# Kernel tuning notes

Hardware: AMD Instinct MI355X
Metric: run time of the kernel (lower is better)

## Reference

```python
import jax, jax.numpy as jnp
import numpy as np

B, S, H = 64, 256, 768
T, D = 13, 64  # ent_type_size, inner_dim
NEG = 1e12


def setup_inputs() -> dict:
    key = jax.random.key(0)
    k1, k2 = jax.random.split(key)
    return {
        "last_hidden_state": jax.random.normal(k1, (B, S, H), dtype=jnp.float32),
        "dense_w": jax.random.normal(k2, (H, T * 2 * D), dtype=jnp.float32) * (1.0 / np.sqrt(H)),
        "dense_b": jnp.zeros((T * 2 * D,), dtype=jnp.float32),
        "attention_mask": jnp.ones((B, S), dtype=jnp.float32),
    }


def _rope_sin_cos(seq_len, dim, dtype):
    # sinusoidal_position_embedding: even slots sin, odd slots cos
    pos = jnp.arange(seq_len, dtype=dtype)[:, None]                      # [S,1]
    inv = jnp.power(10000.0, -2.0 * jnp.arange(dim // 2, dtype=dtype) / dim)
    ang = pos * inv                                                      # [S,D/2]
    # cos_pos = emb[...,1::2].repeat_interleave(2) ; sin_pos = emb[...,::2].repeat_interleave(2)
    cos_pos = jnp.repeat(jnp.cos(ang), 2, axis=-1)                       # [S,D]
    sin_pos = jnp.repeat(jnp.sin(ang), 2, axis=-1)                       # [S,D]
    return sin_pos, cos_pos


def _rotate(x):
    # stack([-x[...,1::2], x[...,::2]], -1).reshape(x.shape)
    x2 = jnp.stack([-x[..., 1::2], x[..., ::2]], axis=-1)
    return x2.reshape(x.shape)


def reference(last_hidden_state, dense_w, dense_b, attention_mask):
    b, s, _ = last_hidden_state.shape
    out = last_hidden_state @ dense_w + dense_b                          # [B,S,T*2D]
    out = out.reshape(b, s, T, 2 * D)                                    # split+stack
    qw, kw = out[..., :D], out[..., D:]                                  # [B,S,T,D]

    sin_pos, cos_pos = _rope_sin_cos(s, D, out.dtype)
    cosb = cos_pos[None, :, None, :]                                     # [1,S,1,D]
    sinb = sin_pos[None, :, None, :]
    qw = qw * cosb + _rotate(qw) * sinb
    kw = kw * cosb + _rotate(kw) * sinb

    logits = jnp.einsum('bmhd,bnhd->bhmn', qw, kw)                       # [B,T,S,S]

    pad = attention_mask[:, None, None, :]                               # mask over key dim n
    logits = logits * pad - (1.0 - pad) * NEG
    tril = jnp.tril(jnp.ones((s, s), dtype=logits.dtype), -1)            # strict lower tri
    logits = logits - tril * NEG
    return logits / (D ** 0.5)
```

## Files before the change

### kernel.cpp

```cpp
#include <hip/hip_runtime.h>

#define S_LEN 256
#define H_DIM 768
#define T_HEADS 13
#define WN 1664
#define NEGV 1.0e12f

typedef __bf16 bf16x8 __attribute__((ext_vector_type(8)));
typedef float f32x4 __attribute__((ext_vector_type(4)));
typedef float f32x16 __attribute__((ext_vector_type(16)));
typedef unsigned int u32x4 __attribute__((ext_vector_type(4)));
typedef int i32x8 __attribute__((ext_vector_type(8)));

static __device__ __forceinline__ ushort f2bf(float x) {
  unsigned u = __float_as_uint(x);
  return (ushort)((u + 0x7FFFu + ((u >> 16) & 1u)) >> 16);
}

#define GLOAD16(gp, lp)                                                        \
  __builtin_amdgcn_global_load_lds(                                            \
      (const __attribute__((address_space(1))) unsigned int*)(gp),             \
      (__attribute__((address_space(3))) unsigned int*)(lp), 16, 0, 0)

#define PREP_LHS_BLOCKS 6144
#define PREP_WT_BLOCKS 312
#define PREP_ROPE_BLOCKS 16

__global__ __launch_bounds__(256) void prep_all(const float* __restrict__ lhs,
                                                const float* __restrict__ W,
                                                unsigned char* __restrict__ lhs8,
                                                unsigned char* __restrict__ wt8,
                                                float2* __restrict__ rope) {
  const int tid = threadIdx.x;
  const unsigned bx = blockIdx.x;
  if (bx < PREP_LHS_BLOCKS) {
    size_t base = ((size_t)bx * 256 + tid) * 8;
    float4 v0 = *reinterpret_cast<const float4*>(lhs + base);
    float4 v1 = *reinterpret_cast<const float4*>(lhs + base + 4);
    int d0 = __builtin_amdgcn_cvt_pk_fp8_f32(v0.x, v0.y, 0, false);
    d0 = __builtin_amdgcn_cvt_pk_fp8_f32(v0.z, v0.w, d0, true);
    int d1 = __builtin_amdgcn_cvt_pk_fp8_f32(v1.x, v1.y, 0, false);
    d1 = __builtin_amdgcn_cvt_pk_fp8_f32(v1.z, v1.w, d1, true);
    uint2 u = make_uint2((unsigned)d0, (unsigned)d1);
    *reinterpret_cast<uint2*>(lhs8 + base) = u;
    return;
  }
  if (bx < PREP_LHS_BLOCKS + PREP_WT_BLOCKS) {
    __shared__ float T[64][68];
    const int blk = bx - PREP_LHS_BLOCKS;
    const int k0 = (blk % 12) * 64, c0 = (blk / 12) * 64;
#pragma unroll
    for (int p = 0; p < 4; ++p) {
      int f = p * 256 + tid;
      int r = f >> 4, cg = f & 15;
      float4 v = *reinterpret_cast<const float4*>(W + (size_t)(k0 + r) * WN + c0 + cg * 4);
      T[r][cg * 4 + 0] = v.x; T[r][cg * 4 + 1] = v.y;
      T[r][cg * 4 + 2] = v.z; T[r][cg * 4 + 3] = v.w;
    }
    __syncthreads();
    const int orow = tid >> 2, kq = tid & 3;
    float tf[16];
#pragma unroll
    for (int j = 0; j < 16; ++j) tf[j] = T[kq * 16 + j][orow];
    int d[4];
#pragma unroll
    for (int q = 0; q < 4; ++q) {
      d[q] = __builtin_amdgcn_cvt_pk_fp8_f32(tf[q * 4], tf[q * 4 + 1], 0, false);
      d[q] = __builtin_amdgcn_cvt_pk_fp8_f32(tf[q * 4 + 2], tf[q * 4 + 3], d[q], true);
    }
    uint4 u = make_uint4((unsigned)d[0], (unsigned)d[1], (unsigned)d[2], (unsigned)d[3]);
    *reinterpret_cast<uint4*>(wt8 + (size_t)(c0 + orow) * H_DIM + k0 + kq * 16) = u;
    return;
  }
  const int blk = bx - (PREP_LHS_BLOCKS + PREP_WT_BLOCKS);
  const int row = blk * 16 + (tid >> 4);
  const int cq = (tid & 15) * 4;
#pragma unroll
  for (int q = 0; q < 4; ++q) {
    int c = cq + q;
    float inv = exp2f(-(float)(c >> 1) * 0.4152410118609203f);
    float sv, cv;
    __sincosf((float)row * inv, &sv, &cv);
    rope[(size_t)row * 64 + c] = make_float2(cv, sv);
  }
}

static __device__ __forceinline__ i32x8 frag8(const unsigned char* base, int row,
                                              int ks, int hi2, int l31) {
  union { u32x4 h[2]; i32x8 v; } u;
  const int u0 = (ks * 4 + hi2 * 2 + 0) ^ (l31 & 7);
  const int u1 = (ks * 4 + hi2 * 2 + 1) ^ (l31 & 7);
  u.h[0] = *reinterpret_cast<const u32x4*>(base + row * 128 + u0 * 16);
  u.h[1] = *reinterpret_cast<const u32x4*>(base + row * 128 + u1 * 16);
  return u.v;
}

__global__ __launch_bounds__(512, 2) void gp_fused(
    const unsigned char* __restrict__ lhs8, const unsigned char* __restrict__ wt8,
    const float* __restrict__ bias, const float2* __restrict__ rope,
    const float* __restrict__ amask, float* __restrict__ out) {
  const int x = blockIdx.x;
  const int xcd = x & 7;
  const int seq = x >> 3;
  const int grp = seq / 52;
  const int loc = seq % 52;
  const int b = (xcd + 8 * grp) * 4 + loc / 13;
  const int th = loc % 13;
  const int bid = b * T_HEADS + th;
  const int tid = threadIdx.x;
  const int w = tid >> 6;
  const int lane = tid & 63;
  const int l31 = lane & 31;
  const int hi2 = lane >> 5;
  const int lr8 = lane >> 3;
  const int lsu = (lane & 7) ^ lr8;

  __shared__ union {
    unsigned char stage[2][49152];
    struct { ushort Q[256][72]; ushort K[256][72]; } p2;
  } sm;

  const unsigned char* Ag = lhs8 + (size_t)b * S_LEN * H_DIM;
  const unsigned char* Wg = wt8 + (size_t)th * 128 * H_DIM;

  f32x16 c2[4];
#pragma unroll
  for (int ni = 0; ni < 4; ++ni) c2[ni] = (f32x16){};

#define STAGE_TILE(t, buf)                                                         \
  do {                                                                             \
    unsigned char* sb_ = sm.stage[buf];                                            \
    _Pragma("unroll") for (int j = 0; j < 4; ++j) {                                \
      const int r0 = w * 32 + j * 8;                                               \
      GLOAD16(Ag + (size_t)(r0 + lr8) * H_DIM + (t) * 128 + lsu * 16,              \
              sb_ + r0 * 128);                                                     \
    }                                                                              \
    _Pragma("unroll") for (int j = 0; j < 2; ++j) {                                \
      const int r0 = w * 16 + j * 8;                                               \
      GLOAD16(Wg + (size_t)(r0 + lr8) * H_DIM + (t) * 128 + lsu * 16,              \
              sb_ + 32768 + r0 * 128);                                             \
    }                                                                              \
  } while (0)

  STAGE_TILE(0, 0);
  __syncthreads();
  int cur = 0;
#pragma unroll 1
  for (int t = 0; t < 6; ++t) {
    if (t + 1 < 6) STAGE_TILE(t + 1, cur ^ 1);
    const unsigned char* sa = sm.stage[cur];
    const unsigned char* sw = sm.stage[cur] + 32768;
#pragma unroll
    for (int ks = 0; ks < 2; ++ks) {
      i32x8 a = frag8(sa, w * 32 + l31, ks, hi2, l31);
#pragma unroll
      for (int ni = 0; ni < 4; ++ni) {
        i32x8 bb = frag8(sw, ni * 32 + l31, ks, hi2, l31);
        c2[ni] = __builtin_amdgcn_mfma_scale_f32_32x32x64_f8f6f4(
            a, bb, c2[ni], 0, 0, 0, 0x7F, 0, 0x7F);
      }
    }
    __syncthreads();
    cur ^= 1;
  }

  float bj2[4];
#pragma unroll
  for (int ni = 0; ni < 4; ++ni) bj2[ni] = bias[th * 128 + ni * 32 + l31];
  const float sgn = (l31 & 1) ? 1.0f : -1.0f;

#pragma unroll
  for (int reg = 0; reg < 16; ++reg) {
    int ml = w * 32 + (reg & 3) + 8 * (reg >> 2) + 4 * hi2;
#pragma unroll
    for (int ni = 0; ni < 2; ++ni) {
      float2 cs = rope[(size_t)ml * 64 + ni * 32 + l31];
      {
        float v = c2[ni][reg] + bj2[ni];
        float o = __shfl_xor(v, 1);
        sm.p2.Q[ml][ni * 32 + l31] = f2bf(v * cs.x + sgn * o * cs.y);
      }
      {
        float v = c2[ni + 2][reg] + bj2[ni + 2];
        float o = __shfl_xor(v, 1);
        sm.p2.K[ml][ni * 32 + l31] = f2bf(v * cs.x + sgn * o * cs.y);
      }
    }
  }
  __syncthreads();

  bf16x8 qf2[4];
#pragma unroll
  for (int ks = 0; ks < 4; ++ks)
    qf2[ks] = *reinterpret_cast<const bf16x8*>(
        &sm.p2.Q[w * 32 + l31][ks * 16 + hi2 * 8]);

  const size_t outbase = (size_t)bid * (S_LEN * (size_t)S_LEN);
#pragma unroll 1
  for (int nt = 0; nt < 8; ++nt) {
    bf16x8 kf2[4];
#pragma unroll
    for (int ks = 0; ks < 4; ++ks)
      kf2[ks] = *reinterpret_cast<const bf16x8*>(
          &sm.p2.K[nt * 32 + l31][ks * 16 + hi2 * 8]);

    const int ncol = nt * 32 + l31;
    const float pad = amask[b * S_LEN + ncol];
    const float sub = (1.0f - pad) * NEGV;

    f32x16 cq = {};
#pragma unroll
    for (int ks = 0; ks < 4; ++ks)
      cq = __builtin_amdgcn_mfma_f32_32x32x16_bf16(qf2[ks], kf2[ks], cq, 0, 0, 0);

#pragma unroll
    for (int reg = 0; reg < 16; ++reg) {
      int m = w * 32 + (reg & 3) + 8 * (reg >> 2) + 4 * hi2;
      float v = cq[reg] * pad - sub;
      if (m > ncol) v -= NEGV;
      __builtin_nontemporal_store(v * 0.125f, &out[outbase + (size_t)m * S_LEN + ncol]);
    }
  }
}

__global__ __launch_bounds__(256, 1) void gp_fallback(
    const float* __restrict__ lhs, const float* __restrict__ Wd,
    const float* __restrict__ bias, const float* __restrict__ amask,
    float* __restrict__ out) {
  const int bid0 = blockIdx.x;
  const int bid = (bid0 & 7) * 104 + (bid0 >> 3);
  const int b = bid / T_HEADS;
  const int th = bid % T_HEADS;
  const int wcol0 = th * 128;
  const int tid = threadIdx.x;
  const int w = tid >> 6;
  const int lane = tid & 63;
  const int lo = lane & 15;
  const int hi = lane >> 4;
  const int l31 = lane & 31;
  const int hi2 = lane >> 5;

  __shared__ union {
    struct { ushort A[256][72]; ushort W[128][72]; } p1;
    struct { ushort Q[256][72]; ushort K[256][72]; } p2;
  } sm;
  __shared__ float mask_s[256];

  mask_s[tid] = amask[b * S_LEN + tid];

  f32x4 acc[4][8];
#pragma unroll
  for (int mi = 0; mi < 4; ++mi)
#pragma unroll
    for (int ni = 0; ni < 8; ++ni) acc[mi][ni] = (f32x4){0.f, 0.f, 0.f, 0.f};

  const float* Ab = lhs + (size_t)b * (S_LEN * H_DIM);
  const int wc4 = tid & 31, wrg = tid >> 5;
  for (int k0 = 0; k0 < H_DIM; k0 += 64) {
#pragma unroll
    for (int p = 0; p < 16; ++p) {
      int f = p * 256 + tid;
      int m = f >> 4, c4 = f & 15;
      float4 v = *reinterpret_cast<const float4*>(Ab + (size_t)m * H_DIM + k0 + c4 * 4);
      *reinterpret_cast<ushort4*>(&sm.p1.A[m][c4 * 4]) =
          make_ushort4(f2bf(v.x), f2bf(v.y), f2bf(v.z), f2bf(v.w));
    }
    {
      ushort wt[8][4];
#pragma unroll
      for (int r8 = 0; r8 < 8; ++r8) {
        float4 v = *reinterpret_cast<const float4*>(
            Wd + (size_t)(k0 + wrg * 8 + r8) * WN + wcol0 + wc4 * 4);
        wt[r8][0] = f2bf(v.x); wt[r8][1] = f2bf(v.y);
        wt[r8][2] = f2bf(v.z); wt[r8][3] = f2bf(v.w);
      }
#pragma unroll
      for (int cc = 0; cc < 4; ++cc) {
        *reinterpret_cast<ushort4*>(&sm.p1.W[wc4 * 4 + cc][wrg * 8]) =
            make_ushort4(wt[0][cc], wt[1][cc], wt[2][cc], wt[3][cc]);
        *reinterpret_cast<ushort4*>(&sm.p1.W[wc4 * 4 + cc][wrg * 8 + 4]) =
            make_ushort4(wt[4][cc], wt[5][cc], wt[6][cc], wt[7][cc]);
      }
    }
    __syncthreads();
#pragma unroll
    for (int kk = 0; kk < 2; ++kk) {
      bf16x8 af[4];
#pragma unroll
      for (int mi = 0; mi < 4; ++mi)
        af[mi] = *reinterpret_cast<const bf16x8*>(&sm.p1.A[w * 64 + mi * 16 + lo][kk * 32 + hi * 8]);
#pragma unroll
      for (int ni = 0; ni < 8; ++ni) {
        bf16x8 bfr = *reinterpret_cast<const bf16x8*>(&sm.p1.W[ni * 16 + lo][kk * 32 + hi * 8]);
#pragma unroll
        for (int mi = 0; mi < 4; ++mi)
          acc[mi][ni] = __builtin_amdgcn_mfma_f32_16x16x32_bf16(af[mi], bfr, acc[mi][ni], 0, 0, 0);
      }
    }
    __syncthreads();
  }

  float bj[8];
#pragma unroll
  for (int ni = 0; ni < 8; ++ni) bj[ni] = bias[wcol0 + ni * 16 + lo];

  float inv_[4];
#pragma unroll
  for (int ii = 0; ii < 4; ++ii)
    inv_[ii] = exp2f(-(float)(ii * 8 + (lo >> 1)) * 0.4152410118609203f);
  const float sgn = (lo & 1) ? 1.0f : -1.0f;

#pragma unroll
  for (int mi = 0; mi < 4; ++mi) {
#pragma unroll
    for (int r = 0; r < 4; ++r) {
      int m = w * 64 + mi * 16 + hi * 4 + r;
#pragma unroll
      for (int ii = 0; ii < 4; ++ii) {
        float sv, cv;
        __sincosf((float)m * inv_[ii], &sv, &cv);
        {
          float v = acc[mi][ii][r] + bj[ii];
          float o = __shfl_xor(v, 1);
          sm.p2.Q[m][ii * 16 + lo] = f2bf(v * cv + sgn * o * sv);
        }
        {
          float v = acc[mi][ii + 4][r] + bj[ii + 4];
          float o = __shfl_xor(v, 1);
          sm.p2.K[m][ii * 16 + lo] = f2bf(v * cv + sgn * o * sv);
        }
      }
    }
  }
  __syncthreads();

  bf16x8 qf2[2][4];
#pragma unroll
  for (int mtile = 0; mtile < 2; ++mtile)
#pragma unroll
    for (int ks = 0; ks < 4; ++ks)
      qf2[mtile][ks] = *reinterpret_cast<const bf16x8*>(
          &sm.p2.Q[w * 64 + mtile * 32 + l31][ks * 16 + hi2 * 8]);

  const size_t outbase = (size_t)bid * (S_LEN * (size_t)S_LEN);
#pragma unroll 1
  for (int nt = 0; nt < 8; ++nt) {
    bf16x8 kf2[4];
#pragma unroll
    for (int ks = 0; ks < 4; ++ks)
      kf2[ks] = *reinterpret_cast<const bf16x8*>(
          &sm.p2.K[nt * 32 + l31][ks * 16 + hi2 * 8]);

    const int ncol = nt * 32 + l31;
    const float pad = mask_s[ncol];
    const float sub = (1.0f - pad) * NEGV;

#pragma unroll
    for (int mtile = 0; mtile < 2; ++mtile) {
      f32x16 cq = {};
#pragma unroll
      for (int ks = 0; ks < 4; ++ks)
        cq = __builtin_amdgcn_mfma_f32_32x32x16_bf16(qf2[mtile][ks], kf2[ks], cq, 0, 0, 0);

#pragma unroll
      for (int reg = 0; reg < 16; ++reg) {
        int m = w * 64 + mtile * 32 + (reg & 3) + 8 * (reg >> 2) + 4 * hi2;
        float v = cq[reg] * pad - sub;
        if (m > ncol) v -= NEGV;
        __builtin_nontemporal_store(v * 0.125f, &out[outbase + (size_t)m * S_LEN + ncol]);
      }
    }
  }
}

extern "C" void kernel_launch(void* const* d_in, const int* in_sizes, int n_in,
                              void* d_out, int out_size, void* d_ws, size_t ws_size,
                              hipStream_t stream) {
  const float* lhs = (const float*)d_in[0];
  const float* Wd = (const float*)d_in[1];
  const float* bias = (const float*)d_in[2];
  const float* amask = (const float*)d_in[3];
  float* out = (float*)d_out;

  const size_t rope_bytes = (size_t)256 * 64 * sizeof(float2);
  const size_t lhs8_bytes = (size_t)64 * S_LEN * H_DIM;
  const size_t wt8_bytes = (size_t)WN * H_DIM;
  const size_t need = rope_bytes + lhs8_bytes + wt8_bytes;

  if (ws_size >= need) {
    float2* rope = (float2*)d_ws;
    unsigned char* lhs8 = (unsigned char*)d_ws + rope_bytes;
    unsigned char* wt8 = lhs8 + lhs8_bytes;
    prep_all<<<dim3(PREP_LHS_BLOCKS + PREP_WT_BLOCKS + PREP_ROPE_BLOCKS), 256, 0, stream>>>(
        lhs, Wd, lhs8, wt8, rope);
    gp_fused<<<dim3(64 * T_HEADS), 512, 0, stream>>>(lhs8, wt8, bias, rope, amask, out);
  } else {
    gp_fallback<<<dim3(64 * T_HEADS), 256, 0, stream>>>(lhs, Wd, bias, amask, out);
  }
}
```

Before: 89.62 us.

## Make fused kernel persistent and overlap next head's projection GEMM with logits stores

The fused kernel now launches 256 persistent blocks, each handling 3 or 4 (batch, head) pairs in sequence instead of one block per pair. While one head's logits tiles are computed and streamed out, the fp8 projection GEMM for the next head is staged and run in the same loop, so store traffic overlaps with the GEMM. The staging buffer is now single-buffered and kept separate from the Q/K tiles, which raises shared memory use and puts two barriers in every tile iteration. Spreading 832 heads over 256 blocks as 3 or 4 each can leave some blocks idle while others finish.

```diff
diff --git a/kernel.cpp b/kernel.cpp
--- a/kernel.cpp
+++ b/kernel.cpp
@@ -101,12 +101,9 @@
     const float* __restrict__ amask, float* __restrict__ out) {
   const int x = blockIdx.x;
   const int xcd = x & 7;
-  const int seq = x >> 3;
-  const int grp = seq / 52;
-  const int loc = seq % 52;
-  const int b = (xcd + 8 * grp) * 4 + loc / 13;
-  const int th = loc % 13;
-  const int bid = b * T_HEADS + th;
+  const int cu = x >> 3;
+  const int hstart = (cu < 8) ? 4 * cu : 32 + 3 * (cu - 8);
+  const int hcnt = (cu < 8) ? 4 : 3;
   const int tid = threadIdx.x;
   const int w = tid >> 6;
   const int lane = tid & 63;
@@ -115,110 +112,143 @@
   const int lr8 = lane >> 3;
   const int lsu = (lane & 7) ^ lr8;
 
-  __shared__ union {
-    unsigned char stage[2][49152];
-    struct { ushort Q[256][72]; ushort K[256][72]; } p2;
+  __shared__ struct {
+    unsigned char stageA[256 * 128];
+    unsigned char stageW[128 * 128];
+    ushort Q[256][72];
+    ushort K[256][72];
   } sm;
 
-  const unsigned char* Ag = lhs8 + (size_t)b * S_LEN * H_DIM;
-  const unsigned char* Wg = wt8 + (size_t)th * 128 * H_DIM;
-
-  f32x16 c2[4];
-#pragma unroll
-  for (int ni = 0; ni < 4; ++ni) c2[ni] = (f32x16){};
-
-#define STAGE_TILE(t, buf)                                                         \
-  do {                                                                             \
-    unsigned char* sb_ = sm.stage[buf];                                            \
-    _Pragma("unroll") for (int j = 0; j < 4; ++j) {                                \
-      const int r0 = w * 32 + j * 8;                                               \
-      GLOAD16(Ag + (size_t)(r0 + lr8) * H_DIM + (t) * 128 + lsu * 16,              \
-              sb_ + r0 * 128);                                                     \
-    }                                                                              \
-    _Pragma("unroll") for (int j = 0; j < 2; ++j) {                                \
-      const int r0 = w * 16 + j * 8;                                               \
-      GLOAD16(Wg + (size_t)(r0 + lr8) * H_DIM + (t) * 128 + lsu * 16,              \
-              sb_ + 32768 + r0 * 128);                                             \
-    }                                                                              \
-  } while (0)
-
-  STAGE_TILE(0, 0);
-  __syncthreads();
-  int cur = 0;
-#pragma unroll 1
-  for (int t = 0; t < 6; ++t) {
-    if (t + 1 < 6) STAGE_TILE(t + 1, cur ^ 1);
-    const unsigned char* sa = sm.stage[cur];
-    const unsigned char* sw = sm.stage[cur] + 32768;
+  auto headBT = [&](int hs, int& b, int& th) {
+    int g = hs / 52, loc = hs % 52;
+    b = (xcd + 8 * g) * 4 + loc / 13;
+    th = loc % 13;
+  };
+
+  auto STAGE = [&](const unsigned char* Ag, const unsigned char* Wg, int t) {
+#pragma unroll
+    for (int jj = 0; jj < 4; ++jj) {
+      const int r0 = w * 32 + jj * 8;
+      GLOAD16(Ag + (size_t)(r0 + lr8) * H_DIM + t * 128 + lsu * 16, &sm.stageA[r0 * 128]);
+    }
+#pragma unroll
+    for (int jj = 0; jj < 2; ++jj) {
+      const int r0 = w * 16 + jj * 8;
+      GLOAD16(Wg + (size_t)(r0 + lr8) * H_DIM + t * 128 + lsu * 16, &sm.stageW[r0 * 128]);
+    }
+  };
+
+  auto GEMM_TILE = [&](f32x16* c2) {
 #pragma unroll
     for (int ks = 0; ks < 2; ++ks) {
-      i32x8 a = frag8(sa, w * 32 + l31, ks, hi2, l31);
+      i32x8 a = frag8(sm.stageA, w * 32 + l31, ks, hi2, l31);
 #pragma unroll
       for (int ni = 0; ni < 4; ++ni) {
-        i32x8 bb = frag8(sw, ni * 32 + l31, ks, hi2, l31);
+        i32x8 bb = frag8(sm.stageW, ni * 32 + l31, ks, hi2, l31);
         c2[ni] = __builtin_amdgcn_mfma_scale_f32_32x32x64_f8f6f4(
             a, bb, c2[ni], 0, 0, 0, 0x7F, 0, 0x7F);
       }
     }
-    __syncthreads();
-    cur ^= 1;
-  }
-
-  float bj2[4];
-#pragma unroll
-  for (int ni = 0; ni < 4; ++ni) bj2[ni] = bias[th * 128 + ni * 32 + l31];
+  };
+
   const float sgn = (l31 & 1) ? 1.0f : -1.0f;
-
-#pragma unroll
-  for (int reg = 0; reg < 16; ++reg) {
-    int ml = w * 32 + (reg & 3) + 8 * (reg >> 2) + 4 * hi2;
-#pragma unroll
-    for (int ni = 0; ni < 2; ++ni) {
-      float2 cs = rope[(size_t)ml * 64 + ni * 32 + l31];
-      {
-        float v = c2[ni][reg] + bj2[ni];
-        float o = __shfl_xor(v, 1);
-        sm.p2.Q[ml][ni * 32 + l31] = f2bf(v * cs.x + sgn * o * cs.y);
-      }
-      {
-        float v = c2[ni + 2][reg] + bj2[ni + 2];
-        float o = __shfl_xor(v, 1);
-        sm.p2.K[ml][ni * 32 + l31] = f2bf(v * cs.x + sgn * o * cs.y);
-      }
-    }
-  }
-  __syncthreads();
-
-  bf16x8 qf2[4];
-#pragma unroll
-  for (int ks = 0; ks < 4; ++ks)
-    qf2[ks] = *reinterpret_cast<const bf16x8*>(
-        &sm.p2.Q[w * 32 + l31][ks * 16 + hi2 * 8]);
-
-  const size_t outbase = (size_t)bid * (S_LEN * (size_t)S_LEN);
-#pragma unroll 1
-  for (int nt = 0; nt < 8; ++nt) {
+  auto PHASE_B = [&](f32x16* c2, int th) {
+    float bj2[4];
+#pragma unroll
+    for (int ni = 0; ni < 4; ++ni) bj2[ni] = bias[th * 128 + ni * 32 + l31];
+#pragma unroll
+    for (int reg = 0; reg < 16; ++reg) {
+      int ml = w * 32 + (reg & 3) + 8 * (reg >> 2) + 4 * hi2;
+#pragma unroll
+      for (int ni = 0; ni < 2; ++ni) {
+        float2 cs = rope[(size_t)ml * 64 + ni * 32 + l31];
+        {
+          float v = c2[ni][reg] + bj2[ni];
+          float o = __shfl_xor(v, 1);
+          sm.Q[ml][ni * 32 + l31] = f2bf(v * cs.x + sgn * o * cs.y);
+        }
+        {
+          float v = c2[ni + 2][reg] + bj2[ni + 2];
+          float o = __shfl_xor(v, 1);
+          sm.K[ml][ni * 32 + l31] = f2bf(v * cs.x + sgn * o * cs.y);
+        }
+      }
+    }
+  };
+
+  auto C_ITER = [&](int nt, int b, size_t outbase, const bf16x8* qf2) {
     bf16x8 kf2[4];
 #pragma unroll
     for (int ks = 0; ks < 4; ++ks)
       kf2[ks] = *reinterpret_cast<const bf16x8*>(
-          &sm.p2.K[nt * 32 + l31][ks * 16 + hi2 * 8]);
-
+          &sm.K[nt * 32 + l31][ks * 16 + hi2 * 8]);
     const int ncol = nt * 32 + l31;
     const float pad = amask[b * S_LEN + ncol];
     const float sub = (1.0f - pad) * NEGV;
-
     f32x16 cq = {};
 #pragma unroll
     for (int ks = 0; ks < 4; ++ks)
       cq = __builtin_amdgcn_mfma_f32_32x32x16_bf16(qf2[ks], kf2[ks], cq, 0, 0, 0);
-
 #pragma unroll
     for (int reg = 0; reg < 16; ++reg) {
       int m = w * 32 + (reg & 3) + 8 * (reg >> 2) + 4 * hi2;
       float v = cq[reg] * pad - sub;
       if (m > ncol) v -= NEGV;
       __builtin_nontemporal_store(v * 0.125f, &out[outbase + (size_t)m * S_LEN + ncol]);
+    }
+  };
+
+  int b, th;
+  headBT(hstart, b, th);
+  const unsigned char* Ag = lhs8 + (size_t)b * S_LEN * H_DIM;
+  const unsigned char* Wg = wt8 + (size_t)th * 128 * H_DIM;
+
+  f32x16 c2[4];
+#pragma unroll
+  for (int ni = 0; ni < 4; ++ni) c2[ni] = (f32x16){};
+#pragma unroll 1
+  for (int t = 0; t < 6; ++t) {
+    STAGE(Ag, Wg, t);
+    __syncthreads();
+    GEMM_TILE(c2);
+    __syncthreads();
+  }
+
+#pragma unroll 1
+  for (int hh = 0; hh < hcnt; ++hh) {
+    headBT(hstart + hh, b, th);
+    const size_t outbase = (size_t)(b * T_HEADS + th) * (S_LEN * (size_t)S_LEN);
+
+    PHASE_B(c2, th);
+    __syncthreads();
+
+    bf16x8 qf2[4];
+#pragma unroll
+    for (int ks = 0; ks < 4; ++ks)
+      qf2[ks] = *reinterpret_cast<const bf16x8*>(
+          &sm.Q[w * 32 + l31][ks * 16 + hi2 * 8]);
+#pragma unroll
+    for (int ni = 0; ni < 4; ++ni) c2[ni] = (f32x16){};
+
+    if (hh + 1 < hcnt) {
+      int bn, thn;
+      headBT(hstart + hh + 1, bn, thn);
+      const unsigned char* Agn = lhs8 + (size_t)bn * S_LEN * H_DIM;
+      const unsigned char* Wgn = wt8 + (size_t)thn * 128 * H_DIM;
+#pragma unroll 1
+      for (int t = 0; t < 6; ++t) {
+        STAGE(Agn, Wgn, t);
+        C_ITER(t, b, outbase, qf2);
+        __syncthreads();
+        GEMM_TILE(c2);
+        __syncthreads();
+      }
+      C_ITER(6, b, outbase, qf2);
+      C_ITER(7, b, outbase, qf2);
+      __syncthreads();
+    } else {
+#pragma unroll 1
+      for (int nt = 0; nt < 8; ++nt) C_ITER(nt, b, outbase, qf2);
     }
   }
 }
@@ -393,7 +423,7 @@
     unsigned char* wt8 = lhs8 + lhs8_bytes;
     prep_all<<<dim3(PREP_LHS_BLOCKS + PREP_WT_BLOCKS + PREP_ROPE_BLOCKS), 256, 0, stream>>>(
         lhs, Wd, lhs8, wt8, rope);
-    gp_fused<<<dim3(64 * T_HEADS), 512, 0, stream>>>(lhs8, wt8, bias, rope, amask, out);
+    gp_fused<<<dim3(256), 512, 0, stream>>>(lhs8, wt8, bias, rope, amask, out);
   } else {
     gp_fallback<<<dim3(64 * T_HEADS), 256, 0, stream>>>(lhs, Wd, bias, amask, out);
   }
```

New measurement: 116.8 us. 30.4% more time.
